# Optimization experiments

Measured on AMD Instinct MI355X. Metric: run time of the kernel, lower is better.

Reference implementation:

```python
import jax, jax.numpy as jnp
import numpy as np
import math

DIM = 4096
N_HEADS = 32
N_KV_HEADS = 8
HEAD_DIM = DIM // N_HEADS          # 128
N_REP = N_HEADS // N_KV_HEADS      # 4
BATCH = 2
SEQ = 2048
ROPE_THETA = 10000.0


def rope_cos_sin(seq_len, head_dim, theta=ROPE_THETA):
    # matches precompute_freqs_cis: freqs over even indices, outer with positions
    inv_freq = 1.0 / (theta ** (jnp.arange(0, head_dim, 2, dtype=jnp.float32) / head_dim))
    t = jnp.arange(seq_len, dtype=jnp.float32)
    ang = jnp.outer(t, inv_freq)          # [S, head_dim//2]
    return jnp.cos(ang), jnp.sin(ang)


def apply_rope(x, cos, sin):
    # x: [B, S, H, D]; consecutive pairs (x0, x1) form complex numbers (view_as_complex)
    x0 = x[..., 0::2]
    x1 = x[..., 1::2]
    c = cos[None, :, None, :]
    s = sin[None, :, None, :]
    r0 = x0 * c - x1 * s
    r1 = x0 * s + x1 * c
    return jnp.stack([r0, r1], axis=-1).reshape(x.shape)


def setup_inputs() -> dict:
    key = jax.random.key(0)
    ks = jax.random.split(key, 5)
    scale = 1.0 / math.sqrt(DIM)
    return {
        "x": jax.random.normal(ks[0], (BATCH, SEQ, DIM), dtype=jnp.float32),
        "wq": jax.random.normal(ks[1], (DIM, N_HEADS * HEAD_DIM), dtype=jnp.float32) * scale,
        "wk": jax.random.normal(ks[2], (DIM, N_KV_HEADS * HEAD_DIM), dtype=jnp.float32) * scale,
        "wv": jax.random.normal(ks[3], (DIM, N_KV_HEADS * HEAD_DIM), dtype=jnp.float32) * scale,
        "wo": jax.random.normal(ks[4], (N_HEADS * HEAD_DIM, DIM), dtype=jnp.float32) * scale,
        "start_pos": 0,
    }


def reference(x, wq, wk, wv, wo, start_pos):
    B, S, _ = x.shape
    # projections
    q = (x @ wq).reshape(B, S, N_HEADS, HEAD_DIM)
    k = (x @ wk).reshape(B, S, N_KV_HEADS, HEAD_DIM)
    v = (x @ wv).reshape(B, S, N_KV_HEADS, HEAD_DIM)
    # RoPE on q, k (training path: full-sequence freqs)
    cos, sin = rope_cos_sin(S, HEAD_DIM)
    q = apply_rope(q, cos, sin)
    k = apply_rope(k, cos, sin)
    # GQA: repeat_kv expands kv heads by n_rep
    k = jnp.repeat(k, N_REP, axis=2)  # [B, S, H, D]
    v = jnp.repeat(v, N_REP, axis=2)
    # [B, H, S, D]
    q = q.transpose(0, 2, 1, 3)
    k = k.transpose(0, 2, 1, 3)
    v = v.transpose(0, 2, 1, 3)
    scores = jnp.einsum("bhqd,bhkd->bhqk", q, k) / math.sqrt(HEAD_DIM)
    # causal mask: -inf above diagonal
    mask = jnp.triu(jnp.full((S, S), float("-inf"), dtype=scores.dtype), k=1)
    scores = scores + mask[None, None]
    attn = jax.nn.softmax(scores.astype(jnp.float32), axis=-1).astype(q.dtype)
    out = jnp.einsum("bhqk,bhkd->bhqd", attn, v)
    out = out.transpose(0, 2, 1, 3).reshape(B, S, N_HEADS * HEAD_DIM)
    return out @ wo
```

## Files before the change

kernel.cpp:

```cpp
#include <hip/hip_runtime.h>

#define DIM 4096
#define HD 128
#define NH 32
#define NKV 8
#define SEQ 2048
#define BATCH 2
#define MTOT (BATCH*SEQ)
#define GK DIM

typedef __bf16 bf16;
typedef __bf16 bf16x4 __attribute__((ext_vector_type(4)));
typedef __bf16 bf16x8 __attribute__((ext_vector_type(8)));
typedef float f32x4 __attribute__((ext_vector_type(4)));

__device__ __forceinline__ void gload_lds16(const void* g, void* l) {
    __builtin_amdgcn_global_load_lds(
        (const __attribute__((address_space(1))) void*)g,
        (__attribute__((address_space(3))) void*)l, 16, 0, 0);
}

__device__ __forceinline__ void tconv64_tile(const float* __restrict__ in,
                                             bf16* __restrict__ out,
                                             int N, int K, int bx, int by,
                                             float t[64][65], int tid) {
    int rr = tid >> 4;
    int cc = (tid & 15) * 4;
    const float* ip = in + ((size_t)(by * 64 + rr)) * N + bx * 64 + cc;
#pragma unroll
    for (int p = 0; p < 4; ++p) {
        float4 v = *(const float4*)(ip + (size_t)p * 16 * N);
        t[rr + p * 16][cc + 0] = v.x;
        t[rr + p * 16][cc + 1] = v.y;
        t[rr + p * 16][cc + 2] = v.z;
        t[rr + p * 16][cc + 3] = v.w;
    }
    __syncthreads();
#pragma unroll
    for (int p = 0; p < 4; ++p) {
        int n = rr + p * 16;
        bf16x4 o;
#pragma unroll
        for (int j = 0; j < 4; ++j) o[j] = (bf16)t[cc + j][n];
        *(bf16x4*)(out + (size_t)(bx * 64 + n) * K + by * 64 + cc) = o;
    }
}

__global__ __launch_bounds__(256) void prep(const float* __restrict__ x,
                                            const float* __restrict__ wq,
                                            const float* __restrict__ wk,
                                            const float* __restrict__ wv,
                                            bf16* __restrict__ xb,
                                            bf16* __restrict__ wqt,
                                            bf16* __restrict__ wkt,
                                            bf16* __restrict__ wvt) {
    __shared__ float t[64][65];
    const int bid = blockIdx.x, tid = threadIdx.x;
    if (bid < 8192) {
        int i = bid * 256 + tid;
        const float4* p = (const float4*)(x + (size_t)i * 8);
        float4 a = p[0], b = p[1];
        bf16x8 v;
        v[0]=(bf16)a.x; v[1]=(bf16)a.y; v[2]=(bf16)a.z; v[3]=(bf16)a.w;
        v[4]=(bf16)b.x; v[5]=(bf16)b.y; v[6]=(bf16)b.z; v[7]=(bf16)b.w;
        *(bf16x8*)(xb + (size_t)i * 8) = v;
    } else if (bid < 8192 + 4096) {
        int b2 = bid - 8192;
        tconv64_tile(wq, wqt, DIM, DIM, b2 & 63, b2 >> 6, t, tid);
    } else if (bid < 8192 + 4096 + 1024) {
        int b2 = bid - (8192 + 4096);
        tconv64_tile(wk, wkt, 1024, DIM, b2 & 15, b2 >> 4, t, tid);
    } else {
        int b2 = bid - (8192 + 4096 + 1024);
        tconv64_tile(wv, wvt, 1024, DIM, b2 & 15, b2 >> 4, t, tid);
    }
}

__global__ __launch_bounds__(256) void tconv64(const float* __restrict__ in,
                                               bf16* __restrict__ out, int N, int K) {
    __shared__ float t[64][65];
    tconv64_tile(in, out, N, K, blockIdx.x, blockIdx.y, t, threadIdx.x);
}

__global__ __launch_bounds__(256) void rope_both(bf16* __restrict__ qb,
                                                 bf16* __restrict__ kb, float qs) {
    const int bid = blockIdx.x, tid = threadIdx.x;
    bf16* buf; int shift; float os; int i;
    if (bid < 8192) { buf = qb; shift = 12; os = qs; i = bid * 256 + tid; }
    else            { buf = kb; shift = 10; os = 1.f; i = (bid - 8192) * 256 + tid; }
    size_t base = (size_t)i * 8;
    int col = (int)(base & ((1u << shift) - 1));
    int pos = (int)((base >> shift) & (SEQ - 1));
    int d0 = col & (HD - 1);
    bf16x8 v = *(const bf16x8*)(buf + base);
    float f[8];
#pragma unroll
    for (int j = 0; j < 8; ++j) f[j] = (float)v[j];
    const float nl2t = -13.287712379549449f / 64.f;
#pragma unroll
    for (int j = 0; j < 4; ++j) {
        float inv = exp2f(nl2t * (float)((d0 >> 1) + j));
        float ang = (float)pos * inv;
        float sn, cs;
        sincosf(ang, &sn, &cs);
        float x0 = f[2 * j], x1 = f[2 * j + 1];
        f[2 * j]     = x0 * cs - x1 * sn;
        f[2 * j + 1] = x0 * sn + x1 * cs;
    }
    bf16x8 ov;
#pragma unroll
    for (int j = 0; j < 8; ++j) ov[j] = (bf16)(f[j] * os);
    *(bf16x8*)(buf + base) = ov;
}

__global__ __launch_bounds__(256) void gemm_kv(const bf16* __restrict__ xb,
                                               const bf16* __restrict__ wkt,
                                               const bf16* __restrict__ wvt,
                                               bf16* __restrict__ kb,
                                               bf16* __restrict__ vtb) {
    __shared__ alignas(16) bf16 sA[2][128 * 32];
    __shared__ alignas(16) bf16 sB[2][128 * 32];
    const int tid = threadIdx.x;
    const int lane = tid & 63, wid = tid >> 6;
    const int wm = wid >> 1, wn = wid & 1;

    const bf16 *A, *Bt;
    bf16* out0;
    int N, m0, n0;
    const int bid = blockIdx.x;
    if (bid < 256) {
        A = xb; Bt = wkt; out0 = kb; N = 1024;
        m0 = (bid >> 3) * 128; n0 = (bid & 7) * 128;
    } else {
        int b2 = bid - 256;
        A = wvt; Bt = xb; out0 = vtb; N = MTOT;
        m0 = (b2 >> 5) * 128; n0 = (b2 & 31) * 128;
    }

    auto stage = [&](int buf, int kt) {
#pragma unroll
        for (int it = 0; it < 2; ++it) {
            int slot = it * 256 + tid;
            int row = slot >> 2, s = slot & 3;
            gload_lds16(A + (size_t)(m0 + row) * GK + kt * 32 + s * 8, &sA[buf][slot * 8]);
            gload_lds16(Bt + (size_t)(n0 + row) * GK + kt * 32 + s * 8, &sB[buf][slot * 8]);
        }
    };

    f32x4 acc[4][4] = {};
    stage(0, 0);
    __syncthreads();
    int cur = 0;
    for (int kt = 0; kt < GK / 32; ++kt) {
        if (kt + 1 < GK / 32) stage(cur ^ 1, kt + 1);
        bf16x8 bF[4], aF[4];
#pragma unroll
        for (int i = 0; i < 4; ++i)
            bF[i] = *(const bf16x8*)&sB[cur][(wn * 64 + i * 16 + (lane & 15)) * 32 + (lane >> 4) * 8];
#pragma unroll
        for (int i = 0; i < 4; ++i)
            aF[i] = *(const bf16x8*)&sA[cur][(wm * 64 + i * 16 + (lane & 15)) * 32 + (lane >> 4) * 8];
#pragma unroll
        for (int mi = 0; mi < 4; ++mi)
#pragma unroll
            for (int ni = 0; ni < 4; ++ni)
                acc[mi][ni] = __builtin_amdgcn_mfma_f32_16x16x32_bf16(aF[mi], bF[ni], acc[mi][ni], 0, 0, 0);
        __syncthreads();
        cur ^= 1;
    }
#pragma unroll
    for (int mi = 0; mi < 4; ++mi)
#pragma unroll
        for (int ni = 0; ni < 4; ++ni)
#pragma unroll
            for (int r = 0; r < 4; ++r) {
                int row = m0 + wm * 64 + mi * 16 + (lane >> 4) * 4 + r;
                int col = n0 + wn * 64 + ni * 16 + (lane & 15);
                out0[(size_t)row * N + col] = (bf16)acc[mi][ni][r];
            }
}

template <bool F32OUT>
__global__ __launch_bounds__(512, 2) void gemm8(const bf16* __restrict__ A,
                                                const bf16* __restrict__ Bt,
                                                void* __restrict__ outp, int N) {
    __shared__ alignas(16) char sA[2][2][16384];
    __shared__ alignas(16) char sB[2][2][16384];
    const int tid = threadIdx.x, lane = tid & 63;
    const int wid = tid >> 6;
    const int wm = wid >> 2, wn = wid & 3;
    const int m0 = blockIdx.y * 256, n0 = blockIdx.x * 256;
    const int lrow = lane & 15, hc = lane >> 4;
    const int rowbase = ((lrow >> 1) * 128) +
                        (((((lrow & 1) << 2) | hc) ^ (lrow >> 1)) << 4);
    const int NT = GK / 64;

    auto stageR = [&](int t, int kh) {
#pragma unroll
        for (int it = 0; it < 2; ++it) {
            int sl = it * 512 + tid;
            int PRr = sl >> 3, ps = sl & 7;
            int lsl = ps ^ (PRr & 7);
            int r = PRr * 2 + (lsl >> 2);
            int cc = lsl & 3;
            size_t koff = (size_t)t * 64 + kh * 32 + cc * 8;
            gload_lds16(A + (size_t)(m0 + r) * GK + koff, &sA[t & 1][kh][sl * 16]);
            gload_lds16(Bt + (size_t)(n0 + r) * GK + koff, &sB[t & 1][kh][sl * 16]);
        }
    };

    f32x4 acc[8][4] = {};
    bf16x8 af[8], bfr[4];

    auto phread = [&](int t, int kh) {
        const char* Ab = &sA[t & 1][kh][0];
        const char* Bb = &sB[t & 1][kh][0];
#pragma unroll
        for (int ni = 0; ni < 4; ++ni)
            bfr[ni] = *(const bf16x8*)(Bb + wn * 4096 + ni * 1024 + rowbase);
#pragma unroll
        for (int mi = 0; mi < 8; ++mi)
            af[mi] = *(const bf16x8*)(Ab + wm * 8192 + mi * 1024 + rowbase);
    };
    auto phmfma = [&]() {
        __builtin_amdgcn_s_barrier();
        asm volatile("" ::: "memory");
        __builtin_amdgcn_s_setprio(1);
#pragma unroll
        for (int mi = 0; mi < 8; ++mi)
#pragma unroll
            for (int ni = 0; ni < 4; ++ni)
                acc[mi][ni] = __builtin_amdgcn_mfma_f32_16x16x32_bf16(af[mi], bfr[ni], acc[mi][ni], 0, 0, 0);
        __builtin_amdgcn_s_setprio(0);
    };

    stageR(0, 0); stageR(0, 1); stageR(1, 0);
    asm volatile("s_waitcnt vmcnt(8)" ::: "memory");
    __builtin_amdgcn_s_barrier();
    asm volatile("" ::: "memory");

    for (int t = 0; t < NT - 2; ++t) {
        phread(t, 0);
        stageR(t + 1, 1);
        asm volatile("s_waitcnt vmcnt(8)" ::: "memory");
        phmfma();
        phread(t, 1);
        stageR(t + 2, 0);
        asm volatile("s_waitcnt vmcnt(8)" ::: "memory");
        phmfma();
    }
    phread(NT - 2, 0);
    stageR(NT - 1, 1);
    asm volatile("s_waitcnt vmcnt(8)" ::: "memory");
    phmfma();
    phread(NT - 2, 1);
    asm volatile("s_waitcnt vmcnt(4)" ::: "memory");
    phmfma();
    phread(NT - 1, 0);
    asm volatile("s_waitcnt vmcnt(0)" ::: "memory");
    phmfma();
    phread(NT - 1, 1);
    phmfma();

#pragma unroll
    for (int mi = 0; mi < 8; ++mi)
#pragma unroll
        for (int ni = 0; ni < 4; ++ni)
#pragma unroll
            for (int r = 0; r < 4; ++r) {
                int row = m0 + wm * 128 + mi * 16 + hc * 4 + r;
                int col = n0 + wn * 64 + ni * 16 + lrow;
                if constexpr (F32OUT)
                    ((float*)outp)[(size_t)row * N + col] = acc[mi][ni][r];
                else
                    ((bf16*)outp)[(size_t)row * N + col] = (bf16)acc[mi][ni][r];
            }
}

__global__ __launch_bounds__(512, 4) void attn_fwd(const bf16* __restrict__ q,
                                                   const bf16* __restrict__ k,
                                                   const bf16* __restrict__ vt,
                                                   bf16* __restrict__ o) {
    __shared__ alignas(16) bf16 sK[2][64 * 128];
    __shared__ alignas(16) bf16 sV[2][128 * 64];
    __shared__ alignas(16) bf16 sP[8][16 * 64];
    const int tid = threadIdx.x, lane = tid & 63, wid = tid >> 6;
    const int bi = blockIdx.x;
    const int pr = bi & 7;
    const int h = (bi >> 3) & 31;
    const int b = bi >> 8;
    const int kvh = h >> 2;

    const bf16* kb0 = k + (size_t)b * SEQ * (NKV * HD) + kvh * HD;
    const bf16* vb0 = vt + (size_t)(kvh * HD) * MTOT + (size_t)b * SEQ;

    auto stage = [&](int bf, int tt) {
#pragma unroll
        for (int it = 0; it < 2; ++it) {
            int slot = it * 512 + tid;
            int row = slot >> 4, s = slot & 15;
            gload_lds16(kb0 + (size_t)(tt * 64 + row) * (NKV * HD) + ((s ^ (row & 7)) * 8),
                        &sK[bf][slot * 8]);
        }
#pragma unroll
        for (int it = 0; it < 2; ++it) {
            int slot = it * 512 + tid;
            int row = slot >> 3, s = slot & 7;
            gload_lds16(vb0 + (size_t)row * MTOT + tt * 64 + ((s ^ (row & 7)) * 8),
                        &sV[bf][slot * 8]);
        }
    };

    auto pass = [&](int qt) {
        const int qb0 = qt * 128;
        const int nt = 2 * qt + 2;
        const int qw = qb0 + wid * 16;
        const bf16* qp = q + ((size_t)(b * SEQ + qw + (lane & 15))) * DIM
                           + h * HD + (lane >> 4) * 8;
        bf16x8 aQ[4];
#pragma unroll
        for (int ks = 0; ks < 4; ++ks) aQ[ks] = *(const bf16x8*)(qp + ks * 32);

        f32x4 accO[8] = {};
        float m_r = -1e30f, l_r = 0.f;
        const int qglob = qw + (lane & 15);
        char* pb = (char*)&sP[wid][0];
        const int q7s = (lane & 7) << 4;
        const int hi = lane >> 4;

        stage(0, 0);
        __syncthreads();
        int cur = 0;
        for (int tt = 0; tt < nt; ++tt) {
            if (tt + 1 < nt) stage(cur ^ 1, tt + 1);
            if (tt * 64 <= qw) {
                f32x4 accS[4] = {};
#pragma unroll
                for (int nt2 = 0; nt2 < 4; ++nt2) {
                    int kr = nt2 * 16 + (lane & 15);
#pragma unroll
                    for (int ks = 0; ks < 4; ++ks) {
                        int slog = ks * 4 + hi;
                        bf16x8 bK = *(const bf16x8*)&sK[cur][kr * 128 + ((slog ^ (kr & 7)) * 8)];
                        accS[nt2] = __builtin_amdgcn_mfma_f32_16x16x32_bf16(bK, aQ[ks], accS[nt2], 0, 0, 0);
                    }
                }

                const bool diag = (tt * 64 + 63 > qw);
                float mx = -1e30f;
                if (diag) {
                    const int kvb = tt * 64 + hi * 4;
#pragma unroll
                    for (int nt2 = 0; nt2 < 4; ++nt2)
#pragma unroll
                        for (int r = 0; r < 4; ++r) {
                            float v = accS[nt2][r];
                            if (kvb + nt2 * 16 + r > qglob) v = -1e30f;
                            accS[nt2][r] = v;
                            mx = fmaxf(mx, v);
                        }
                } else {
#pragma unroll
                    for (int nt2 = 0; nt2 < 4; ++nt2)
#pragma unroll
                        for (int r = 0; r < 4; ++r) mx = fmaxf(mx, accS[nt2][r]);
                }
                mx = fmaxf(mx, __shfl_xor(mx, 16, 64));
                mx = fmaxf(mx, __shfl_xor(mx, 32, 64));

                if (!__all(mx <= m_r + 8.f)) {
                    float mn = fmaxf(m_r, mx);
                    float al = __builtin_amdgcn_exp2f(m_r - mn);
                    m_r = mn;
                    l_r *= al;
                    float al4[4];
#pragma unroll
                    for (int r = 0; r < 4; ++r) al4[r] = __shfl(al, hi * 4 + r, 64);
#pragma unroll
                    for (int d2 = 0; d2 < 8; ++d2)
#pragma unroll
                        for (int r = 0; r < 4; ++r) accO[d2][r] *= al4[r];
                }

                float rs = 0.f;
#pragma unroll
                for (int nt2 = 0; nt2 < 4; ++nt2)
#pragma unroll
                    for (int r = 0; r < 4; ++r) {
                        float p = __builtin_amdgcn_exp2f(accS[nt2][r] - m_r);
                        accS[nt2][r] = p;
                        rs += p;
                    }
                rs += __shfl_xor(rs, 16, 64);
                rs += __shfl_xor(rs, 32, 64);
                l_r += rs;

#pragma unroll
                for (int nt2 = 0; nt2 < 4; ++nt2) {
                    bf16x4 pv;
                    pv[0] = (bf16)accS[nt2][0]; pv[1] = (bf16)accS[nt2][1];
                    pv[2] = (bf16)accS[nt2][2]; pv[3] = (bf16)accS[nt2][3];
                    *(bf16x4*)(pb + (lane & 15) * 128 + ((nt2 * 32 + hi * 8) ^ q7s)) = pv;
                }

                bf16x8 aP[2];
#pragma unroll
                for (int kk = 0; kk < 2; ++kk)
                    aP[kk] = *(const bf16x8*)(pb + (lane & 15) * 128 + ((kk * 64 + hi * 16) ^ q7s));
#pragma unroll
                for (int d2 = 0; d2 < 8; ++d2) {
#pragma unroll
                    for (int kk = 0; kk < 2; ++kk) {
                        int dv = d2 * 16 + (lane & 15);
                        int phys = (kk * 4 + hi) ^ (dv & 7);
                        bf16x8 bV = *(const bf16x8*)&sV[cur][dv * 64 + phys * 8];
                        accO[d2] = __builtin_amdgcn_mfma_f32_16x16x32_bf16(aP[kk], bV, accO[d2], 0, 0, 0);
                    }
                }
            }
            __syncthreads();
            cur ^= 1;
        }

        float linv[4];
#pragma unroll
        for (int r = 0; r < 4; ++r) linv[r] = 1.f / __shfl(l_r, hi * 4 + r, 64);
        size_t orow = (size_t)(b * SEQ + qb0 + wid * 16 + hi * 4) * DIM
                    + h * HD + (lane & 15);
#pragma unroll
        for (int d2 = 0; d2 < 8; ++d2)
#pragma unroll
            for (int r = 0; r < 4; ++r)
                o[orow + (size_t)r * DIM + d2 * 16] = (bf16)(accO[d2][r] * linv[r]);
    };

    pass(pr);
    pass(15 - pr);
}

extern "C" void kernel_launch(void* const* d_in, const int* in_sizes, int n_in,
                              void* d_out, int out_size, void* d_ws, size_t ws_size,
                              hipStream_t stream) {
    const float* x  = (const float*)d_in[0];
    const float* wq = (const float*)d_in[1];
    const float* wk = (const float*)d_in[2];
    const float* wv = (const float*)d_in[3];
    const float* wo = (const float*)d_in[4];
    float* out = (float*)d_out;

    char* ws = (char*)d_ws;
    size_t off = 0;
    bf16* xb  = (bf16*)(ws + off); off += (size_t)MTOT * DIM * 2;
    bf16* wqt = (bf16*)(ws + off); off += (size_t)DIM * DIM * 2;
    bf16* wkt = (bf16*)(ws + off); off += (size_t)1024 * DIM * 2;
    bf16* wvt = (bf16*)(ws + off); off += (size_t)1024 * DIM * 2;
    bf16* qb  = (bf16*)(ws + off); off += (size_t)MTOT * DIM * 2;
    bf16* kb  = (bf16*)(ws + off); off += (size_t)MTOT * 1024 * 2;
    bf16* vtb = (bf16*)(ws + off); off += (size_t)MTOT * 1024 * 2;
    bf16* ao = xb;

    const float SCALE2 = 0.08838834764831845f * 1.44269504088896340f;

    prep<<<8192 + 4096 + 1024 + 1024, 256, 0, stream>>>(x, wq, wk, wv, xb, wqt, wkt, wvt);

    gemm8<false><<<dim3(DIM / 256, MTOT / 256), 512, 0, stream>>>(xb, wqt, qb, DIM);
    gemm_kv<<<512, 256, 0, stream>>>(xb, wkt, wvt, kb, vtb);

    rope_both<<<8192 + 2048, 256, 0, stream>>>(qb, kb, SCALE2);

    tconv64<<<dim3(DIM / 64, DIM / 64), 256, 0, stream>>>(wo, wqt, DIM, DIM);

    attn_fwd<<<BATCH * NH * 8, 512, 0, stream>>>(qb, kb, vtb, ao);

    gemm8<true><<<dim3(DIM / 256, MTOT / 256), 512, 0, stream>>>(ao, wqt, out, DIM);
}
```

Before: 531.3 us.

## Split GEMM k-phase into two half-M MFMA clusters with interleaved LDS reads

New measurement: 546.9 us. +2.9%, slower.

```diff
diff --git a/kernel.cpp b/kernel.cpp
--- a/kernel.cpp
+++ b/kernel.cpp
@@ -210,57 +210,60 @@
     };
 
     f32x4 acc[8][4] = {};
-    bf16x8 af[8], bfr[4];
-
-    auto phread = [&](int t, int kh) {
+
+    auto region = [&](int t, int kh, int st, int sh, int vm, bool dostage) {
         const char* Ab = &sA[t & 1][kh][0];
         const char* Bb = &sB[t & 1][kh][0];
+        bf16x8 af[4], bfr[4];
 #pragma unroll
         for (int ni = 0; ni < 4; ++ni)
             bfr[ni] = *(const bf16x8*)(Bb + wn * 4096 + ni * 1024 + rowbase);
 #pragma unroll
-        for (int mi = 0; mi < 8; ++mi)
+        for (int mi = 0; mi < 4; ++mi)
             af[mi] = *(const bf16x8*)(Ab + wm * 8192 + mi * 1024 + rowbase);
-    };
-    auto phmfma = [&]() {
+        if (dostage) stageR(st, sh);
+        if (vm == 8)      asm volatile("s_waitcnt vmcnt(8)" ::: "memory");
+        else if (vm == 4) asm volatile("s_waitcnt vmcnt(4)" ::: "memory");
+        else if (vm == 0) asm volatile("s_waitcnt vmcnt(0)" ::: "memory");
         __builtin_amdgcn_s_barrier();
-        asm volatile("" ::: "memory");
+        asm volatile("s_waitcnt lgkmcnt(0)" ::: "memory");
+        __builtin_amdgcn_sched_barrier(0);
         __builtin_amdgcn_s_setprio(1);
 #pragma unroll
-        for (int mi = 0; mi < 8; ++mi)
+        for (int mi = 0; mi < 4; ++mi)
 #pragma unroll
             for (int ni = 0; ni < 4; ++ni)
                 acc[mi][ni] = __builtin_amdgcn_mfma_f32_16x16x32_bf16(af[mi], bfr[ni], acc[mi][ni], 0, 0, 0);
         __builtin_amdgcn_s_setprio(0);
+        __builtin_amdgcn_s_barrier();
+#pragma unroll
+        for (int mi = 0; mi < 4; ++mi)
+            af[mi] = *(const bf16x8*)(Ab + wm * 8192 + (4 + mi) * 1024 + rowbase);
+        __builtin_amdgcn_s_barrier();
+        asm volatile("s_waitcnt lgkmcnt(0)" ::: "memory");
+        __builtin_amdgcn_sched_barrier(0);
+        __builtin_amdgcn_s_setprio(1);
+#pragma unroll
+        for (int mi = 0; mi < 4; ++mi)
+#pragma unroll
+            for (int ni = 0; ni < 4; ++ni)
+                acc[4 + mi][ni] = __builtin_amdgcn_mfma_f32_16x16x32_bf16(af[mi], bfr[ni], acc[4 + mi][ni], 0, 0, 0);
+        __builtin_amdgcn_s_setprio(0);
+        __builtin_amdgcn_s_barrier();
     };
 
     stageR(0, 0); stageR(0, 1); stageR(1, 0);
     asm volatile("s_waitcnt vmcnt(8)" ::: "memory");
     __builtin_amdgcn_s_barrier();
-    asm volatile("" ::: "memory");
 
     for (int t = 0; t < NT - 2; ++t) {
-        phread(t, 0);
-        stageR(t + 1, 1);
-        asm volatile("s_waitcnt vmcnt(8)" ::: "memory");
-        phmfma();
-        phread(t, 1);
-        stageR(t + 2, 0);
-        asm volatile("s_waitcnt vmcnt(8)" ::: "memory");
-        phmfma();
-    }
-    phread(NT - 2, 0);
-    stageR(NT - 1, 1);
-    asm volatile("s_waitcnt vmcnt(8)" ::: "memory");
-    phmfma();
-    phread(NT - 2, 1);
-    asm volatile("s_waitcnt vmcnt(4)" ::: "memory");
-    phmfma();
-    phread(NT - 1, 0);
-    asm volatile("s_waitcnt vmcnt(0)" ::: "memory");
-    phmfma();
-    phread(NT - 1, 1);
-    phmfma();
+        region(t, 0, t + 1, 1, 8, true);
+        region(t, 1, t + 2, 0, 8, true);
+    }
+    region(NT - 2, 0, NT - 1, 1, 8, true);
+    region(NT - 2, 1, 0, 0, 4, false);
+    region(NT - 1, 0, 0, 0, 0, false);
+    region(NT - 1, 1, 0, 0, -1, false);
 
 #pragma unroll
     for (int mi = 0; mi < 8; ++mi)
```

## Fuse RoPE into Q and K projection GEMM epilogues, simplify gemm8 pipeline

Applied to the files above, without the earlier changes.

Result: slower. 1.643 ms (+209.2%).

```diff
diff --git a/kernel.cpp b/kernel.cpp
--- a/kernel.cpp
+++ b/kernel.cpp
@@ -13,6 +13,8 @@
 typedef __bf16 bf16x4 __attribute__((ext_vector_type(4)));
 typedef __bf16 bf16x8 __attribute__((ext_vector_type(8)));
 typedef float f32x4 __attribute__((ext_vector_type(4)));
+
+#define NL2T (-13.287712379549449f / 64.f)
 
 __device__ __forceinline__ void gload_lds16(const void* g, void* l) {
     __builtin_amdgcn_global_load_lds(
@@ -82,37 +84,6 @@
     tconv64_tile(in, out, N, K, blockIdx.x, blockIdx.y, t, threadIdx.x);
 }
 
-__global__ __launch_bounds__(256) void rope_both(bf16* __restrict__ qb,
-                                                 bf16* __restrict__ kb, float qs) {
-    const int bid = blockIdx.x, tid = threadIdx.x;
-    bf16* buf; int shift; float os; int i;
-    if (bid < 8192) { buf = qb; shift = 12; os = qs; i = bid * 256 + tid; }
-    else            { buf = kb; shift = 10; os = 1.f; i = (bid - 8192) * 256 + tid; }
-    size_t base = (size_t)i * 8;
-    int col = (int)(base & ((1u << shift) - 1));
-    int pos = (int)((base >> shift) & (SEQ - 1));
-    int d0 = col & (HD - 1);
-    bf16x8 v = *(const bf16x8*)(buf + base);
-    float f[8];
-#pragma unroll
-    for (int j = 0; j < 8; ++j) f[j] = (float)v[j];
-    const float nl2t = -13.287712379549449f / 64.f;
-#pragma unroll
-    for (int j = 0; j < 4; ++j) {
-        float inv = exp2f(nl2t * (float)((d0 >> 1) + j));
-        float ang = (float)pos * inv;
-        float sn, cs;
-        sincosf(ang, &sn, &cs);
-        float x0 = f[2 * j], x1 = f[2 * j + 1];
-        f[2 * j]     = x0 * cs - x1 * sn;
-        f[2 * j + 1] = x0 * sn + x1 * cs;
-    }
-    bf16x8 ov;
-#pragma unroll
-    for (int j = 0; j < 8; ++j) ov[j] = (bf16)(f[j] * os);
-    *(bf16x8*)(buf + base) = ov;
-}
-
 __global__ __launch_bounds__(256) void gemm_kv(const bf16* __restrict__ xb,
                                                const bf16* __restrict__ wkt,
                                                const bf16* __restrict__ wvt,
@@ -128,7 +99,8 @@
     bf16* out0;
     int N, m0, n0;
     const int bid = blockIdx.x;
-    if (bid < 256) {
+    const bool isK = (bid < 256);
+    if (isK) {
         A = xb; Bt = wkt; out0 = kb; N = 1024;
         m0 = (bid >> 3) * 128; n0 = (bid & 7) * 128;
     } else {
@@ -168,22 +140,51 @@
         __syncthreads();
         cur ^= 1;
     }
-#pragma unroll
-    for (int mi = 0; mi < 4; ++mi)
-#pragma unroll
-        for (int ni = 0; ni < 4; ++ni)
-#pragma unroll
-            for (int r = 0; r < 4; ++r) {
-                int row = m0 + wm * 64 + mi * 16 + (lane >> 4) * 4 + r;
-                int col = n0 + wn * 64 + ni * 16 + (lane & 15);
-                out0[(size_t)row * N + col] = (bf16)acc[mi][ni][r];
-            }
-}
-
-template <bool F32OUT>
+
+    const int lrow = lane & 15;
+    if (isK) {
+        float inv4[4];
+#pragma unroll
+        for (int ni = 0; ni < 4; ++ni) {
+            int d = (wn * 64 + ni * 16 + lrow) & 127;
+            inv4[ni] = exp2f(NL2T * (float)(d >> 1));
+        }
+        const bool ev = (lrow & 1) == 0;
+#pragma unroll
+        for (int mi = 0; mi < 4; ++mi)
+#pragma unroll
+            for (int ni = 0; ni < 4; ++ni)
+#pragma unroll
+                for (int r = 0; r < 4; ++r) {
+                    int row = m0 + wm * 64 + mi * 16 + (lane >> 4) * 4 + r;
+                    int col = n0 + wn * 64 + ni * 16 + lrow;
+                    float v = acc[mi][ni][r];
+                    float p = __shfl_xor(v, 1, 64);
+                    float ang = (float)(row & (SEQ - 1)) * inv4[ni];
+                    float sn, cs;
+                    sincosf(ang, &sn, &cs);
+                    float o = v * cs + (ev ? -p * sn : p * sn);
+                    out0[(size_t)row * N + col] = (bf16)o;
+                }
+    } else {
+#pragma unroll
+        for (int mi = 0; mi < 4; ++mi)
+#pragma unroll
+            for (int ni = 0; ni < 4; ++ni)
+#pragma unroll
+                for (int r = 0; r < 4; ++r) {
+                    int row = m0 + wm * 64 + mi * 16 + (lane >> 4) * 4 + r;
+                    int col = n0 + wn * 64 + ni * 16 + lrow;
+                    out0[(size_t)row * N + col] = (bf16)acc[mi][ni][r];
+                }
+    }
+}
+
+template <int MODE>
 __global__ __launch_bounds__(512, 2) void gemm8(const bf16* __restrict__ A,
                                                 const bf16* __restrict__ Bt,
-                                                void* __restrict__ outp, int N) {
+                                                void* __restrict__ outp, int N,
+                                                float oscale) {
     __shared__ alignas(16) char sA[2][2][16384];
     __shared__ alignas(16) char sB[2][2][16384];
     const int tid = threadIdx.x, lane = tid & 63;
@@ -224,7 +225,8 @@
     };
     auto phmfma = [&]() {
         __builtin_amdgcn_s_barrier();
-        asm volatile("" ::: "memory");
+        asm volatile("s_waitcnt lgkmcnt(0)" ::: "memory");
+        __builtin_amdgcn_sched_barrier(0);
         __builtin_amdgcn_s_setprio(1);
 #pragma unroll
         for (int mi = 0; mi < 8; ++mi)
@@ -234,47 +236,63 @@
         __builtin_amdgcn_s_setprio(0);
     };
 
-    stageR(0, 0); stageR(0, 1); stageR(1, 0);
-    asm volatile("s_waitcnt vmcnt(8)" ::: "memory");
+    stageR(0, 0); stageR(0, 1);
+    asm volatile("s_waitcnt vmcnt(4)" ::: "memory");
     __builtin_amdgcn_s_barrier();
-    asm volatile("" ::: "memory");
-
-    for (int t = 0; t < NT - 2; ++t) {
-        phread(t, 0);
-        stageR(t + 1, 1);
-        asm volatile("s_waitcnt vmcnt(8)" ::: "memory");
-        phmfma();
-        phread(t, 1);
-        stageR(t + 2, 0);
-        asm volatile("s_waitcnt vmcnt(8)" ::: "memory");
-        phmfma();
-    }
-    phread(NT - 2, 0);
-    stageR(NT - 1, 1);
-    asm volatile("s_waitcnt vmcnt(8)" ::: "memory");
-    phmfma();
-    phread(NT - 2, 1);
-    asm volatile("s_waitcnt vmcnt(4)" ::: "memory");
-    phmfma();
-    phread(NT - 1, 0);
-    asm volatile("s_waitcnt vmcnt(0)" ::: "memory");
-    phmfma();
-    phread(NT - 1, 1);
-    phmfma();
-
-#pragma unroll
-    for (int mi = 0; mi < 8; ++mi)
-#pragma unroll
-        for (int ni = 0; ni < 4; ++ni)
-#pragma unroll
-            for (int r = 0; r < 4; ++r) {
-                int row = m0 + wm * 128 + mi * 16 + hc * 4 + r;
-                int col = n0 + wn * 64 + ni * 16 + lrow;
-                if constexpr (F32OUT)
-                    ((float*)outp)[(size_t)row * N + col] = acc[mi][ni][r];
-                else
-                    ((bf16*)outp)[(size_t)row * N + col] = (bf16)acc[mi][ni][r];
+
+    for (int t = 0; t < NT; ++t) {
+#pragma unroll
+        for (int kh = 0; kh < 2; ++kh) {
+            phread(t, kh);
+            if (t + 1 < NT) {
+                stageR(t + 1, kh);
+                asm volatile("s_waitcnt vmcnt(4)" ::: "memory");
+            } else {
+                asm volatile("s_waitcnt vmcnt(0)" ::: "memory");
             }
+            phmfma();
+        }
+    }
+
+    if constexpr (MODE == 1) {
+        float inv4[4];
+#pragma unroll
+        for (int ni = 0; ni < 4; ++ni) {
+            int d = ((wn & 1) * 64 + ni * 16 + lrow) & 127;
+            inv4[ni] = exp2f(NL2T * (float)(d >> 1));
+        }
+        const bool ev = (lrow & 1) == 0;
+#pragma unroll
+        for (int mi = 0; mi < 8; ++mi)
+#pragma unroll
+            for (int ni = 0; ni < 4; ++ni)
+#pragma unroll
+                for (int r = 0; r < 4; ++r) {
+                    int row = m0 + wm * 128 + mi * 16 + hc * 4 + r;
+                    int col = n0 + wn * 64 + ni * 16 + lrow;
+                    float v = acc[mi][ni][r];
+                    float p = __shfl_xor(v, 1, 64);
+                    float ang = (float)(row & (SEQ - 1)) * inv4[ni];
+                    float sn, cs;
+                    sincosf(ang, &sn, &cs);
+                    float o = v * cs + (ev ? -p * sn : p * sn);
+                    ((bf16*)outp)[(size_t)row * N + col] = (bf16)(o * oscale);
+                }
+    } else {
+#pragma unroll
+        for (int mi = 0; mi < 8; ++mi)
+#pragma unroll
+            for (int ni = 0; ni < 4; ++ni)
+#pragma unroll
+                for (int r = 0; r < 4; ++r) {
+                    int row = m0 + wm * 128 + mi * 16 + hc * 4 + r;
+                    int col = n0 + wn * 64 + ni * 16 + lrow;
+                    if constexpr (MODE == 2)
+                        ((float*)outp)[(size_t)row * N + col] = acc[mi][ni][r];
+                    else
+                        ((bf16*)outp)[(size_t)row * N + col] = (bf16)acc[mi][ni][r];
+                }
+    }
 }
 
 __global__ __launch_bounds__(512, 4) void attn_fwd(const bf16* __restrict__ q,
@@ -463,14 +481,12 @@
 
     prep<<<8192 + 4096 + 1024 + 1024, 256, 0, stream>>>(x, wq, wk, wv, xb, wqt, wkt, wvt);
 
-    gemm8<false><<<dim3(DIM / 256, MTOT / 256), 512, 0, stream>>>(xb, wqt, qb, DIM);
+    gemm8<1><<<dim3(DIM / 256, MTOT / 256), 512, 0, stream>>>(xb, wqt, qb, DIM, SCALE2);
     gemm_kv<<<512, 256, 0, stream>>>(xb, wkt, wvt, kb, vtb);
 
-    rope_both<<<8192 + 2048, 256, 0, stream>>>(qb, kb, SCALE2);
-
     tconv64<<<dim3(DIM / 64, DIM / 64), 256, 0, stream>>>(wo, wqt, DIM, DIM);
 
     attn_fwd<<<BATCH * NH * 8, 512, 0, stream>>>(qb, kb, vtb, ao);
 
-    gemm8<true><<<dim3(DIM / 256, MTOT / 256), 512, 0, stream>>>(ao, wqt, out, DIM);
-}
+    gemm8<2><<<dim3(DIM / 256, MTOT / 256), 512, 0, stream>>>(ao, wqt, out, DIM, 1.0f);
+}
```
